# Performance work log

Measured on AMD Instinct MI355X. Metric: run time of the kernel, lower is better.

The kernel has to match this reference:

```python
import jax, jax.numpy as jnp
import numpy as np

# e2m1 FP4 lookup table (MXFP4)
FP4_VALUES = jnp.array([0.0, 0.5, 1.0, 1.5, 2.0, 3.0, 4.0, 6.0,
                        -0.0, -0.5, -1.0, -1.5, -2.0, -3.0, -4.0, -6.0], dtype=jnp.float32)
BLOCK = 32  # MXFP4/MXFP8 block size
SWIGLU_LIMIT = 7.0
SWIGLU_ALPHA = 1.702


def mxfp8_qdq(x):
    """Quantize-dequantize x to MXFP8: fp8_e4m3 mantissas with per-32-block E8M0 scales."""
    shp = x.shape
    nb = shp[-1] // BLOCK
    xb = x.reshape(*shp[:-1], nb, BLOCK)
    max_abs = jnp.max(jnp.abs(xb), axis=-1, keepdims=True)
    e = jnp.clip(jnp.ceil(jnp.log2(jnp.maximum(max_abs, 1e-12))), -127.0, 128.0)
    scale = jnp.exp2(e)
    xq = (xb / scale).astype(jnp.float8_e4m3fn).astype(x.dtype) * scale
    return xq.reshape(shp)


def dequant_mxfp4(blocks, scales):
    """blocks: [..., g, 16] int (packed nibbles), scales: [..., g] int (E8M0 biased 127).
    Returns [..., g*32] float32, low nibble first within each byte."""
    lo = FP4_VALUES[blocks & 15]
    hi = FP4_VALUES[blocks >> 4]
    vals = jnp.stack([lo, hi], axis=-1).reshape(*blocks.shape[:-1], BLOCK)  # interleave lo,hi
    e = (scales - 127).astype(jnp.float32)
    w = vals * jnp.exp2(e)[..., None]
    return w.reshape(*blocks.shape[:-2], blocks.shape[-2] * BLOCK)


def moe_forward(hidden_states, expert_indices, routing_weights,
                gate_up_blocks, gate_up_scales, gate_up_bias,
                down_blocks, down_scales, down_bias):
    w_gu = dequant_mxfp4(gate_up_blocks, gate_up_scales)  # [E, 2I, H]
    w_d = dequant_mxfp4(down_blocks, down_scales)          # [E, H, I]
    xq = mxfp8_qdq(hidden_states)                          # [T, H] mxfp8 qdq (row-blockwise)

    def one_expert(wgu, bgu, wd, bd):
        h = xq @ wgu.T + bgu                               # [T, 2I]
        gate = jnp.minimum(h[..., 0::2], SWIGLU_LIMIT)     # interleaved gate/up
        up = jnp.clip(h[..., 1::2], -SWIGLU_LIMIT, SWIGLU_LIMIT)
        glu = gate * jax.nn.sigmoid(SWIGLU_ALPHA * gate)
        act = (up + 1.0) * glu                             # [T, I]
        return mxfp8_qdq(act) @ wd.T + bd                  # [T, H]

    expert_outs = jax.vmap(one_expert)(w_gu, gate_up_bias, w_d, down_bias)  # [E, T, H]
    T = hidden_states.shape[0]
    sel = expert_outs[expert_indices, jnp.arange(T)[:, None]]  # [T, K, H]
    return jnp.sum(routing_weights[..., None] * sel, axis=1)   # [T, H]


def setup_inputs() -> dict:
    key = jax.random.key(0)
    ks = jax.random.split(key, 9)
    E, T, K, H, I = 8, 1024, 2, 2880, 2880
    return {
        'hidden_states': jax.random.normal(ks[0], (T, H), dtype=jnp.float32),
        'expert_indices': jax.random.randint(ks[1], (T, K), 0, E, dtype=jnp.int32),
        'routing_weights': jax.random.uniform(ks[2], (T, K), dtype=jnp.float32),
        'gate_up_blocks': jax.random.randint(ks[3], (E, 2 * I, H // 32, 16), 0, 256, dtype=jnp.int32),
        'gate_up_scales': jax.random.randint(ks[4], (E, 2 * I, H // 32), 0, 132, dtype=jnp.int32),
        'gate_up_bias': jax.random.normal(ks[5], (E, 2 * I), dtype=jnp.float32),
        'down_blocks': jax.random.randint(ks[6], (E, H, I // 32, 16), 0, 256, dtype=jnp.int32),
        'down_scales': jax.random.randint(ks[7], (E, H, I // 32), 0, 132, dtype=jnp.int32),
        'down_bias': jax.random.normal(ks[8], (E, H), dtype=jnp.float32),
    }


def reference(hidden_states, expert_indices, routing_weights,
              gate_up_blocks, gate_up_scales, gate_up_bias,
              down_blocks, down_scales, down_bias):
    return moe_forward(hidden_states, expert_indices, routing_weights,
                       gate_up_blocks, gate_up_scales, gate_up_bias,
                       down_blocks, down_scales, down_bias)
```

## Files before the change

kernel.cpp:

```cpp
#include <hip/hip_runtime.h>
#include <math.h>

#define T_TOK 1024
#define E_EXP 8
#define H_DIM 2880
#define I_DIM 2880
#define NGU   5760
#define KB    90
#define TM 128
#define TN 128
#define MAXROWS 3072

typedef __attribute__((ext_vector_type(8))) short short8;
typedef __attribute__((ext_vector_type(4))) float f32x4;

#define XQ_OFF   0ull
#define ACT_OFF  5898240ull
#define RTOK_OFF 23592960ull
#define RW_OFF   23605248ull
#define EB_OFF   23617536ull
#define EPC_OFF  23617600ull

__device__ inline ushort f2bf(float f) {
  unsigned u = __float_as_uint(f);
  unsigned r = u + 0x7FFFu + ((u >> 16) & 1u);
  return (ushort)(r >> 16);
}

__device__ inline int blk_exp(float amax) {
  amax = fmaxf(amax, 1e-12f);
  unsigned b = __float_as_uint(amax);
  int e = (int)(b >> 23) - 127;
  if (b & 0x7FFFFFu) e += 1;
  return min(max(e, -127), 128);
}

__device__ inline float qdq_val(float v, int eblk) {
  float av = fabsf(v);
  if (av == 0.f) return 0.f;
  int fl = (int)(__float_as_uint(av) >> 23) - 127 - eblk;
  int p = max(fl, -6) - 3;
  float step = ldexpf(1.f, p + eblk);
  return rintf(v / step) * step;
}

__device__ inline float fp4v(int n) {
  int mag = n & 7;
  float v;
  if (mag == 0) v = 0.f;
  else if (mag == 1) v = 0.5f;
  else v = ldexpf(1.0f + 0.5f * (float)(mag & 1), (mag >> 1) - 1);
  return (n & 8) ? -v : v;
}

__global__ void quant_x_kernel(const float* __restrict__ x, ushort* __restrict__ xq) {
  int g = blockIdx.x * 256 + threadIdx.x;
  float4 v4 = ((const float4*)x)[g];
  float am = fmaxf(fmaxf(fabsf(v4.x), fabsf(v4.y)), fmaxf(fabsf(v4.z), fabsf(v4.w)));
  am = fmaxf(am, __shfl_xor(am, 1));
  am = fmaxf(am, __shfl_xor(am, 2));
  am = fmaxf(am, __shfl_xor(am, 4));
  int eb = blk_exp(am);
  ushort4 o;
  o.x = f2bf(qdq_val(v4.x, eb));
  o.y = f2bf(qdq_val(v4.y, eb));
  o.z = f2bf(qdq_val(v4.z, eb));
  o.w = f2bf(qdq_val(v4.w, eb));
  ((ushort4*)xq)[g] = o;
}

__global__ void routing_kernel(const int* __restrict__ eidx, const float* __restrict__ rwt,
                               int* __restrict__ rtok, float* __restrict__ rw,
                               int* __restrict__ ebase, int* __restrict__ epc) {
  __shared__ int cnt[E_EXP];
  __shared__ int base_s[E_EXP];
  __shared__ int pos[E_EXP];
  int t = threadIdx.x;
  if (t < E_EXP) cnt[t] = 0;
  __syncthreads();
  for (int p = t; p < T_TOK * 2; p += 256) atomicAdd(&cnt[eidx[p]], 1);
  __syncthreads();
  if (t == 0) {
    int b = 0;
    for (int e = 0; e < E_EXP; e++) {
      base_s[e] = b;
      b += ((cnt[e] + TM - 1) / TM) * TM;
    }
  }
  __syncthreads();
  if (t < E_EXP) {
    pos[t] = 0;
    ebase[t] = base_s[t];
    epc[t] = ((cnt[t] + TM - 1) / TM) * TM;
  }
  __syncthreads();
  for (int p = t; p < T_TOK * 2; p += 256) {
    int e = eidx[p];
    int o = atomicAdd(&pos[e], 1);
    rtok[base_s[e] + o] = p >> 1;
    rw[base_s[e] + o] = rwt[p];
  }
  __syncthreads();
  for (int e = 0; e < E_EXP; e++) {
    int c = cnt[e], pc = ((c + TM - 1) / TM) * TM;
    for (int i = c + t; i < pc; i += 256) {
      rtok[base_s[e] + i] = 0;
      rw[base_s[e] + i] = 0.f;
    }
  }
}

__global__ __launch_bounds__(256, 2)
void gemm1_kernel(const ushort* __restrict__ xq,
                  const int* __restrict__ gub, const int* __restrict__ gus,
                  const float* __restrict__ gubias,
                  const int* __restrict__ rtok, const int* __restrict__ ebase,
                  const int* __restrict__ epc,
                  ushort* __restrict__ act) {
  const int ntile = blockIdx.x;
  const int e = blockIdx.y >> 4;
  const int mtile = blockIdx.y & 15;
  if (mtile * TM >= epc[e]) return;
  const int rowbase = ebase[e] + mtile * TM;

  __shared__ __align__(16) ushort lA[TM][40];
  __shared__ __align__(16) ushort lB[TN][40];
  __shared__ float2 lut[256];

  const int tid = threadIdx.x;
  lut[tid] = make_float2(fp4v(tid & 15), fp4v((tid >> 4) & 15));
  __syncthreads();

  const int wave = tid >> 6, lane = tid & 63;
  const int half = tid & 1, srow = tid >> 1;
  const int wm = (wave & 1) * 64, wn = (wave >> 1) * 64;
  const int lrow = lane & 15, q = lane >> 4;

  const int tokA = rtok[rowbase + srow];
  const ushort* aSrc = xq + tokA * H_DIM + half * 16;
  const int nrow = ntile * TN + srow;
  const int* bSrc = gub + ((e * NGU + nrow) * KB) * 16 + half * 8;
  const int* sSrc = gus + (e * NGU + nrow) * KB;

  f32x4 acc[4][4];
#pragma unroll
  for (int i = 0; i < 4; i++)
#pragma unroll
    for (int j = 0; j < 4; j++) acc[i][j] = (f32x4){0.f, 0.f, 0.f, 0.f};

  for (int kb = 0; kb < KB; kb++) {
    uint4 a0 = ((const uint4*)(aSrc + kb * 32))[0];
    uint4 a1 = ((const uint4*)(aSrc + kb * 32))[1];
    int4 b0 = ((const int4*)(bSrc + kb * 16))[0];
    int4 b1 = ((const int4*)(bSrc + kb * 16))[1];
    float sc = ldexpf(1.f, sSrc[kb] - 127);

    int bv[8] = {b0.x, b0.y, b0.z, b0.w, b1.x, b1.y, b1.z, b1.w};
    uint us[8];
#pragma unroll
    for (int j = 0; j < 8; j++) {
      float2 l = lut[bv[j] & 255];
      us[j] = (uint)f2bf(l.x * sc) | ((uint)f2bf(l.y * sc) << 16);
    }
    __syncthreads();
    *(uint4*)&lA[srow][half * 16] = a0;
    *(uint4*)&lA[srow][half * 16 + 8] = a1;
    uint4 w0; w0.x = us[0]; w0.y = us[1]; w0.z = us[2]; w0.w = us[3];
    uint4 w1; w1.x = us[4]; w1.y = us[5]; w1.z = us[6]; w1.w = us[7];
    *(uint4*)&lB[srow][half * 16] = w0;
    *(uint4*)&lB[srow][half * 16 + 8] = w1;
    __syncthreads();

    short8 af[4], bfr[4];
#pragma unroll
    for (int mi = 0; mi < 4; mi++) af[mi] = *(const short8*)&lA[wm + mi * 16 + lrow][q * 8];
#pragma unroll
    for (int ni = 0; ni < 4; ni++) bfr[ni] = *(const short8*)&lB[wn + ni * 16 + lrow][q * 8];
#pragma unroll
    for (int mi = 0; mi < 4; mi++)
#pragma unroll
      for (int ni = 0; ni < 4; ni++)
        acc[mi][ni] = __builtin_amdgcn_mfma_f32_16x16x32_bf16(af[mi], bfr[ni], acc[mi][ni], 0, 0, 0);
  }

  const int nbase = ntile * TN + wn;
  float bias_v[4];
#pragma unroll
  for (int ni = 0; ni < 4; ni++) bias_v[ni] = gubias[e * NGU + nbase + ni * 16 + lrow];
  const bool evenl = (lane & 1) == 0;
#pragma unroll
  for (int mi = 0; mi < 4; mi++) {
    float av[4][4];
#pragma unroll
    for (int ni = 0; ni < 4; ni++)
#pragma unroll
      for (int r = 0; r < 4; r++) {
        float h = acc[mi][ni][r] + bias_v[ni];
        float pp = __shfl_xor(h, 1);
        float gate = evenl ? h : pp;
        float up = evenl ? pp : h;
        gate = fminf(gate, 7.f);
        up = fminf(fmaxf(up, -7.f), 7.f);
        float glu = gate / (1.f + expf(-1.702f * gate));
        av[ni][r] = (up + 1.f) * glu;
      }
#pragma unroll
    for (int r = 0; r < 4; r++) {
      float am = 0.f;
#pragma unroll
      for (int ni = 0; ni < 4; ni++) am = fmaxf(am, fabsf(av[ni][r]));
      am = fmaxf(am, __shfl_xor(am, 2));
      am = fmaxf(am, __shfl_xor(am, 4));
      am = fmaxf(am, __shfl_xor(am, 8));
      int eb = blk_exp(am);
      if (evenl) {
        int row = rowbase + wm + mi * 16 + q * 4 + r;
        int cb = (nbase >> 1) + (lrow >> 1);
#pragma unroll
        for (int ni = 0; ni < 4; ni++)
          act[row * I_DIM + cb + ni * 8] = f2bf(qdq_val(av[ni][r], eb));
      }
    }
  }
}

__global__ __launch_bounds__(256, 2)
void gemm2_kernel(const ushort* __restrict__ act,
                  const int* __restrict__ db, const int* __restrict__ dsc,
                  const float* __restrict__ dbias,
                  const int* __restrict__ rtok, const float* __restrict__ rw,
                  const int* __restrict__ ebase, const int* __restrict__ epc,
                  float* __restrict__ out) {
  const int ntile = blockIdx.x;
  const int e = blockIdx.y >> 4;
  const int mtile = blockIdx.y & 15;
  if (mtile * TM >= epc[e]) return;
  const int rowbase = ebase[e] + mtile * TM;

  __shared__ __align__(16) ushort lA[TM][40];
  __shared__ __align__(16) ushort lB[TN][40];
  __shared__ float2 lut[256];

  const int tid = threadIdx.x;
  lut[tid] = make_float2(fp4v(tid & 15), fp4v((tid >> 4) & 15));
  __syncthreads();

  const int wave = tid >> 6, lane = tid & 63;
  const int half = tid & 1, srow = tid >> 1;
  const int wm = (wave & 1) * 64, wn = (wave >> 1) * 64;
  const int lrow = lane & 15, q = lane >> 4;

  const ushort* aSrc = act + (rowbase + srow) * I_DIM + half * 16;
  int nrow = ntile * TN + srow;
  if (nrow >= H_DIM) nrow = H_DIM - 1;
  const int* bSrc = db + ((e * H_DIM + nrow) * KB) * 16 + half * 8;
  const int* sSrc = dsc + (e * H_DIM + nrow) * KB;

  f32x4 acc[4][4];
#pragma unroll
  for (int i = 0; i < 4; i++)
#pragma unroll
    for (int j = 0; j < 4; j++) acc[i][j] = (f32x4){0.f, 0.f, 0.f, 0.f};

  for (int kb = 0; kb < KB; kb++) {
    uint4 a0 = ((const uint4*)(aSrc + kb * 32))[0];
    uint4 a1 = ((const uint4*)(aSrc + kb * 32))[1];
    int4 b0 = ((const int4*)(bSrc + kb * 16))[0];
    int4 b1 = ((const int4*)(bSrc + kb * 16))[1];
    float sc = ldexpf(1.f, sSrc[kb] - 127);

    int bv[8] = {b0.x, b0.y, b0.z, b0.w, b1.x, b1.y, b1.z, b1.w};
    uint us[8];
#pragma unroll
    for (int j = 0; j < 8; j++) {
      float2 l = lut[bv[j] & 255];
      us[j] = (uint)f2bf(l.x * sc) | ((uint)f2bf(l.y * sc) << 16);
    }
    __syncthreads();
    *(uint4*)&lA[srow][half * 16] = a0;
    *(uint4*)&lA[srow][half * 16 + 8] = a1;
    uint4 w0; w0.x = us[0]; w0.y = us[1]; w0.z = us[2]; w0.w = us[3];
    uint4 w1; w1.x = us[4]; w1.y = us[5]; w1.z = us[6]; w1.w = us[7];
    *(uint4*)&lB[srow][half * 16] = w0;
    *(uint4*)&lB[srow][half * 16 + 8] = w1;
    __syncthreads();

    short8 af[4], bfr[4];
#pragma unroll
    for (int mi = 0; mi < 4; mi++) af[mi] = *(const short8*)&lA[wm + mi * 16 + lrow][q * 8];
#pragma unroll
    for (int ni = 0; ni < 4; ni++) bfr[ni] = *(const short8*)&lB[wn + ni * 16 + lrow][q * 8];
#pragma unroll
    for (int mi = 0; mi < 4; mi++)
#pragma unroll
      for (int ni = 0; ni < 4; ni++)
        acc[mi][ni] = __builtin_amdgcn_mfma_f32_16x16x32_bf16(af[mi], bfr[ni], acc[mi][ni], 0, 0, 0);
  }

  const int nbase = ntile * TN + wn;
  float bias_v[4];
#pragma unroll
  for (int ni = 0; ni < 4; ni++) {
    int n = nbase + ni * 16 + lrow;
    bias_v[ni] = (n < H_DIM) ? dbias[e * H_DIM + n] : 0.f;
  }
#pragma unroll
  for (int mi = 0; mi < 4; mi++)
#pragma unroll
    for (int r = 0; r < 4; r++) {
      int orow = rowbase + wm + mi * 16 + q * 4 + r;
      int tok = rtok[orow];
      float w = rw[orow];
      if (w != 0.f) {
#pragma unroll
        for (int ni = 0; ni < 4; ni++) {
          int n = nbase + ni * 16 + lrow;
          if (n < H_DIM) atomicAdd(&out[tok * H_DIM + n], w * (acc[mi][ni][r] + bias_v[ni]));
        }
      }
    }
}

extern "C" void kernel_launch(void* const* d_in, const int* in_sizes, int n_in,
                              void* d_out, int out_size, void* d_ws, size_t ws_size,
                              hipStream_t stream) {
  const float* hs = (const float*)d_in[0];
  const int* eidx = (const int*)d_in[1];
  const float* rwt = (const float*)d_in[2];
  const int* gub = (const int*)d_in[3];
  const int* gus = (const int*)d_in[4];
  const float* gubias = (const float*)d_in[5];
  const int* db = (const int*)d_in[6];
  const int* dsc = (const int*)d_in[7];
  const float* dbias = (const float*)d_in[8];
  float* out = (float*)d_out;
  char* ws = (char*)d_ws;

  ushort* xq = (ushort*)(ws + XQ_OFF);
  ushort* act = (ushort*)(ws + ACT_OFF);
  int* rtok = (int*)(ws + RTOK_OFF);
  float* rw = (float*)(ws + RW_OFF);
  int* ebase = (int*)(ws + EB_OFF);
  int* epc = (int*)(ws + EPC_OFF);

  hipMemsetAsync(d_out, 0, (size_t)out_size * sizeof(float), stream);
  quant_x_kernel<<<2880, 256, 0, stream>>>(hs, xq);
  routing_kernel<<<1, 256, 0, stream>>>(eidx, rwt, rtok, rw, ebase, epc);
  gemm1_kernel<<<dim3(45, 128), 256, 0, stream>>>(xq, gub, gus, gubias, rtok, ebase, epc, act);
  gemm2_kernel<<<dim3(23, 128), 256, 0, stream>>>(act, db, dsc, dbias, rtok, rw, ebase, epc, out);
}
```

Before: 922.4 us.

## Prefetch next K-block into registers, simplify FP4 decode, split-K gemm2

Both GEMM kernels now load the next K-block's activations, packed weights and scale into registers while the current block is decoded and multiplied, to hide global load latency. FP4 decode packs bf16 halves with a byte permute instead of the f2bf conversion; this is exact because FP4 values times power-of-two scales fit in bf16. gemm2 is split along K into two halves via a third grid dimension, with bias added only by the first half, to raise parallelism for the small down-projection grid. The split doubles atomic adds to the output and register pressure rises from the prefetch buffers.

Result: faster. 810.4 us (-12.1%).

```diff
diff --git a/kernel.cpp b/kernel.cpp
--- a/kernel.cpp
+++ b/kernel.cpp
@@ -51,6 +51,13 @@
   else if (mag == 1) v = 0.5f;
   else v = ldexpf(1.0f + 0.5f * (float)(mag & 1), (mag >> 1) - 1);
   return (n & 8) ? -v : v;
+}
+
+__device__ inline uint dec_byte(const float2* lut, int b, float sc) {
+  float2 l = lut[b & 255];
+  uint lo = __float_as_uint(l.x * sc);
+  uint hi = __float_as_uint(l.y * sc);
+  return __builtin_amdgcn_perm(hi, lo, 0x07060302u);
 }
 
 __global__ void quant_x_kernel(const float* __restrict__ x, ushort* __restrict__ xq) {
@@ -148,20 +155,31 @@
 #pragma unroll
     for (int j = 0; j < 4; j++) acc[i][j] = (f32x4){0.f, 0.f, 0.f, 0.f};
 
+  uint4 a0 = ((const uint4*)(aSrc))[0];
+  uint4 a1 = ((const uint4*)(aSrc))[1];
+  int4 b0 = ((const int4*)(bSrc))[0];
+  int4 b1 = ((const int4*)(bSrc))[1];
+  int sraw = sSrc[0];
+
   for (int kb = 0; kb < KB; kb++) {
-    uint4 a0 = ((const uint4*)(aSrc + kb * 32))[0];
-    uint4 a1 = ((const uint4*)(aSrc + kb * 32))[1];
-    int4 b0 = ((const int4*)(bSrc + kb * 16))[0];
-    int4 b1 = ((const int4*)(bSrc + kb * 16))[1];
-    float sc = ldexpf(1.f, sSrc[kb] - 127);
-
-    int bv[8] = {b0.x, b0.y, b0.z, b0.w, b1.x, b1.y, b1.z, b1.w};
+    const int nk = (kb + 1 < KB) ? kb + 1 : kb;
+    uint4 na0 = ((const uint4*)(aSrc + nk * 32))[0];
+    uint4 na1 = ((const uint4*)(aSrc + nk * 32))[1];
+    int4 nb0 = ((const int4*)(bSrc + nk * 16))[0];
+    int4 nb1 = ((const int4*)(bSrc + nk * 16))[1];
+    int nsraw = sSrc[nk];
+
+    float sc = ldexpf(1.f, sraw - 127);
     uint us[8];
-#pragma unroll
-    for (int j = 0; j < 8; j++) {
-      float2 l = lut[bv[j] & 255];
-      us[j] = (uint)f2bf(l.x * sc) | ((uint)f2bf(l.y * sc) << 16);
-    }
+    us[0] = dec_byte(lut, b0.x, sc);
+    us[1] = dec_byte(lut, b0.y, sc);
+    us[2] = dec_byte(lut, b0.z, sc);
+    us[3] = dec_byte(lut, b0.w, sc);
+    us[4] = dec_byte(lut, b1.x, sc);
+    us[5] = dec_byte(lut, b1.y, sc);
+    us[6] = dec_byte(lut, b1.z, sc);
+    us[7] = dec_byte(lut, b1.w, sc);
+
     __syncthreads();
     *(uint4*)&lA[srow][half * 16] = a0;
     *(uint4*)&lA[srow][half * 16 + 8] = a1;
@@ -181,6 +199,8 @@
 #pragma unroll
       for (int ni = 0; ni < 4; ni++)
         acc[mi][ni] = __builtin_amdgcn_mfma_f32_16x16x32_bf16(af[mi], bfr[ni], acc[mi][ni], 0, 0, 0);
+
+    a0 = na0; a1 = na1; b0 = nb0; b1 = nb1; sraw = nsraw;
   }
 
   const int nbase = ntile * TN + wn;
@@ -236,6 +256,8 @@
   const int mtile = blockIdx.y & 15;
   if (mtile * TM >= epc[e]) return;
   const int rowbase = ebase[e] + mtile * TM;
+  const int kz = blockIdx.z;
+  const int kb0 = kz * (KB / 2), kb1 = kb0 + (KB / 2);
 
   __shared__ __align__(16) ushort lA[TM][40];
   __shared__ __align__(16) ushort lB[TN][40];
@@ -262,20 +284,31 @@
 #pragma unroll
     for (int j = 0; j < 4; j++) acc[i][j] = (f32x4){0.f, 0.f, 0.f, 0.f};
 
-  for (int kb = 0; kb < KB; kb++) {
-    uint4 a0 = ((const uint4*)(aSrc + kb * 32))[0];
-    uint4 a1 = ((const uint4*)(aSrc + kb * 32))[1];
-    int4 b0 = ((const int4*)(bSrc + kb * 16))[0];
-    int4 b1 = ((const int4*)(bSrc + kb * 16))[1];
-    float sc = ldexpf(1.f, sSrc[kb] - 127);
-
-    int bv[8] = {b0.x, b0.y, b0.z, b0.w, b1.x, b1.y, b1.z, b1.w};
+  uint4 a0 = ((const uint4*)(aSrc + kb0 * 32))[0];
+  uint4 a1 = ((const uint4*)(aSrc + kb0 * 32))[1];
+  int4 b0 = ((const int4*)(bSrc + kb0 * 16))[0];
+  int4 b1 = ((const int4*)(bSrc + kb0 * 16))[1];
+  int sraw = sSrc[kb0];
+
+  for (int kb = kb0; kb < kb1; kb++) {
+    const int nk = (kb + 1 < kb1) ? kb + 1 : kb;
+    uint4 na0 = ((const uint4*)(aSrc + nk * 32))[0];
+    uint4 na1 = ((const uint4*)(aSrc + nk * 32))[1];
+    int4 nb0 = ((const int4*)(bSrc + nk * 16))[0];
+    int4 nb1 = ((const int4*)(bSrc + nk * 16))[1];
+    int nsraw = sSrc[nk];
+
+    float sc = ldexpf(1.f, sraw - 127);
     uint us[8];
-#pragma unroll
-    for (int j = 0; j < 8; j++) {
-      float2 l = lut[bv[j] & 255];
-      us[j] = (uint)f2bf(l.x * sc) | ((uint)f2bf(l.y * sc) << 16);
-    }
+    us[0] = dec_byte(lut, b0.x, sc);
+    us[1] = dec_byte(lut, b0.y, sc);
+    us[2] = dec_byte(lut, b0.z, sc);
+    us[3] = dec_byte(lut, b0.w, sc);
+    us[4] = dec_byte(lut, b1.x, sc);
+    us[5] = dec_byte(lut, b1.y, sc);
+    us[6] = dec_byte(lut, b1.z, sc);
+    us[7] = dec_byte(lut, b1.w, sc);
+
     __syncthreads();
     *(uint4*)&lA[srow][half * 16] = a0;
     *(uint4*)&lA[srow][half * 16 + 8] = a1;
@@ -295,6 +328,8 @@
 #pragma unroll
       for (int ni = 0; ni < 4; ni++)
         acc[mi][ni] = __builtin_amdgcn_mfma_f32_16x16x32_bf16(af[mi], bfr[ni], acc[mi][ni], 0, 0, 0);
+
+    a0 = na0; a1 = na1; b0 = nb0; b1 = nb1; sraw = nsraw;
   }
 
   const int nbase = ntile * TN + wn;
@@ -302,7 +337,7 @@
 #pragma unroll
   for (int ni = 0; ni < 4; ni++) {
     int n = nbase + ni * 16 + lrow;
-    bias_v[ni] = (n < H_DIM) ? dbias[e * H_DIM + n] : 0.f;
+    bias_v[ni] = (kz == 0 && n < H_DIM) ? dbias[e * H_DIM + n] : 0.f;
   }
 #pragma unroll
   for (int mi = 0; mi < 4; mi++)
@@ -347,5 +382,5 @@
   quant_x_kernel<<<2880, 256, 0, stream>>>(hs, xq);
   routing_kernel<<<1, 256, 0, stream>>>(eidx, rwt, rtok, rw, ebase, epc);
   gemm1_kernel<<<dim3(45, 128), 256, 0, stream>>>(xq, gub, gus, gubias, rtok, ebase, epc, act);
-  gemm2_kernel<<<dim3(23, 128), 256, 0, stream>>>(act, db, dsc, dbias, rtok, rw, ebase, epc, out);
-}
+  gemm2_kernel<<<dim3(23, 128, 2), 256, 0, stream>>>(act, db, dsc, dbias, rtok, rw, ebase, epc, out);
+}
```

## Repack int32 MXFP4 weights to bytes, decode via byte-permute tables, split-K gemm2

Applied to the files above, without the earlier changes.

Adds a repack pass that compresses the int32-per-byte weight and scale arrays into packed bytes, so the GEMM kernels read a quarter of the weight traffic. New gemm kernels decode FP4 nibbles to bf16 by truncation with v_perm table lookups instead of an LDS LUT plus rounding, and register-prefetch the next K step. gemm2 is split along K in two halves combined through the existing atomics. The repack runs on every call, and bf16 truncation is exact only because the scaled FP4 values fit in bf16.

Result: faster. 816.6 us (-11.5%).

```diff
diff --git a/kernel.cpp b/kernel.cpp
--- a/kernel.cpp
+++ b/kernel.cpp
@@ -14,12 +14,19 @@
 typedef __attribute__((ext_vector_type(8))) short short8;
 typedef __attribute__((ext_vector_type(4))) float f32x4;
 
+#define PERM(a, b, s) __builtin_amdgcn_perm((uint)(a), (uint)(b), (uint)(s))
+
 #define XQ_OFF   0ull
 #define ACT_OFF  5898240ull
 #define RTOK_OFF 23592960ull
 #define RW_OFF   23605248ull
 #define EB_OFF   23617536ull
-#define EPC_OFF  23617600ull
+#define EPC_OFF  23617568ull
+#define CGU_OFF  23617664ull
+#define CGS_OFF  89972864ull
+#define CDB_OFF  94120064ull
+#define CDS_OFF  127297664ull
+#define WS_NEED  129371264ull
 
 __device__ inline ushort f2bf(float f) {
   unsigned u = __float_as_uint(f);
@@ -51,6 +58,75 @@
   else if (mag == 1) v = 0.5f;
   else v = ldexpf(1.0f + 0.5f * (float)(mag & 1), (mag >> 1) - 1);
   return (n & 8) ? -v : v;
+}
+
+__device__ inline uint dec_byte(const float2* lut, int b, float sc) {
+  float2 l = lut[b & 255];
+  uint lo = __float_as_uint(l.x * sc);
+  uint hi = __float_as_uint(l.y * sc);
+  return PERM(hi, lo, 0x07060302u);
+}
+
+struct BTbl { uint tlo_l, tlo_h, thi_l, thi_h; };
+
+__device__ inline BTbl build_tbl(float sc) {
+  uint g0 = 0u;
+  uint g1 = __float_as_uint(0.5f * sc);
+  uint g2 = __float_as_uint(sc);
+  uint g3 = __float_as_uint(1.5f * sc);
+  uint g4 = __float_as_uint(2.0f * sc);
+  uint g5 = __float_as_uint(3.0f * sc);
+  uint g6 = __float_as_uint(4.0f * sc);
+  uint g7 = __float_as_uint(6.0f * sc);
+  uint p01 = PERM(g1, g0, 0x07030602u);
+  uint p23 = PERM(g3, g2, 0x07030602u);
+  uint p45 = PERM(g5, g4, 0x07030602u);
+  uint p67 = PERM(g7, g6, 0x07030602u);
+  BTbl t;
+  t.tlo_l = PERM(p23, p01, 0x05040100u);
+  t.thi_l = PERM(p23, p01, 0x07060302u);
+  t.tlo_h = PERM(p67, p45, 0x05040100u);
+  t.thi_h = PERM(p67, p45, 0x07060302u);
+  return t;
+}
+
+__device__ inline uint4 dec_w(uint w, const BTbl& t) {
+  uint ml = w & 0x07070707u;
+  uint mh = (w >> 4) & 0x07070707u;
+  uint sl = (w << 4) & 0x80808080u;
+  uint sh = w & 0x80808080u;
+  uint hl = PERM(t.thi_h, t.thi_l, ml) | sl;
+  uint hh = PERM(t.thi_h, t.thi_l, mh) | sh;
+  uint ll = PERM(t.tlo_h, t.tlo_l, ml);
+  uint lh = PERM(t.tlo_h, t.tlo_l, mh);
+  uint4 o;
+  o.x = PERM(hl, ll, 0x05010400u);
+  o.y = PERM(hl, ll, 0x07030602u);
+  o.z = PERM(hh, lh, 0x05010400u);
+  o.w = PERM(hh, lh, 0x07030602u);
+  return o;
+}
+
+__device__ inline uint4 aperm(uint4 u) {
+  uint4 v;
+  v.x = PERM(u.y, u.x, 0x05040100u);
+  v.y = PERM(u.w, u.z, 0x05040100u);
+  v.z = PERM(u.y, u.x, 0x07060302u);
+  v.w = PERM(u.w, u.z, 0x07060302u);
+  return v;
+}
+
+__global__ void repack_kernel(const int* __restrict__ src, uint4* __restrict__ dst, int n16) {
+  int g = blockIdx.x * 256 + threadIdx.x;
+  if (g >= n16) return;
+  const int4* s = (const int4*)(src) + g * 4;
+  int4 w0 = s[0], w1 = s[1], w2 = s[2], w3 = s[3];
+  uint4 o;
+  o.x = (uint)(w0.x & 255) | ((uint)(w0.y & 255) << 8) | ((uint)(w0.z & 255) << 16) | ((uint)(w0.w) << 24);
+  o.y = (uint)(w1.x & 255) | ((uint)(w1.y & 255) << 8) | ((uint)(w1.z & 255) << 16) | ((uint)(w1.w) << 24);
+  o.z = (uint)(w2.x & 255) | ((uint)(w2.y & 255) << 8) | ((uint)(w2.z & 255) << 16) | ((uint)(w2.w) << 24);
+  o.w = (uint)(w3.x & 255) | ((uint)(w3.y & 255) << 8) | ((uint)(w3.z & 255) << 16) | ((uint)(w3.w) << 24);
+  dst[g] = o;
 }
 
 __global__ void quant_x_kernel(const float* __restrict__ x, ushort* __restrict__ xq) {
@@ -111,6 +187,221 @@
 }
 
 __global__ __launch_bounds__(256, 2)
+void gemm1c_kernel(const ushort* __restrict__ xq,
+                   const uchar* __restrict__ cgu, const uchar* __restrict__ cgs,
+                   const float* __restrict__ gubias,
+                   const int* __restrict__ rtok, const int* __restrict__ ebase,
+                   const int* __restrict__ epc,
+                   ushort* __restrict__ act) {
+  const int ntile = blockIdx.x;
+  const int e = blockIdx.y >> 4;
+  const int mtile = blockIdx.y & 15;
+  if (mtile * TM >= epc[e]) return;
+  const int rowbase = ebase[e] + mtile * TM;
+
+  __shared__ __align__(16) ushort lA[TM][40];
+  __shared__ __align__(16) ushort lB[TN][40];
+
+  const int tid = threadIdx.x;
+  const int wave = tid >> 6, lane = tid & 63;
+  const int half = tid & 1, srow = tid >> 1;
+  const int wm = (wave & 1) * 64, wn = (wave >> 1) * 64;
+  const int lrow = lane & 15, q = lane >> 4;
+
+  const int tokA = rtok[rowbase + srow];
+  const ushort* aSrc = xq + tokA * H_DIM + half * 16;
+  const int nrow = ntile * TN + srow;
+  const uchar* bSrc = cgu + (size_t)(e * NGU + nrow) * 1440 + half * 8;
+  const uchar* sSrc = cgs + (size_t)(e * NGU + nrow) * KB;
+
+  f32x4 acc[4][4];
+#pragma unroll
+  for (int i = 0; i < 4; i++)
+#pragma unroll
+    for (int j = 0; j < 4; j++) acc[i][j] = (f32x4){0.f, 0.f, 0.f, 0.f};
+
+  uint4 a0 = ((const uint4*)(aSrc))[0];
+  uint4 a1 = ((const uint4*)(aSrc))[1];
+  uint2 bw = *(const uint2*)(bSrc);
+  uchar sb = sSrc[0];
+
+  for (int kb = 0; kb < KB; kb++) {
+    const int nk = (kb + 1 < KB) ? kb + 1 : kb;
+    uint4 na0 = ((const uint4*)(aSrc + nk * 32))[0];
+    uint4 na1 = ((const uint4*)(aSrc + nk * 32))[1];
+    uint2 nbw = *(const uint2*)(bSrc + nk * 16);
+    uchar nsb = sSrc[nk];
+
+    float sc = ldexpf(1.f, (int)sb - 127);
+    BTbl t = build_tbl(sc);
+    uint4 d0 = dec_w(bw.x, t);
+    uint4 d1 = dec_w(bw.y, t);
+    uint4 pa0 = aperm(a0);
+    uint4 pa1 = aperm(a1);
+
+    __syncthreads();
+    *(uint4*)&lA[srow][half * 16] = pa0;
+    *(uint4*)&lA[srow][half * 16 + 8] = pa1;
+    *(uint4*)&lB[srow][half * 16] = d0;
+    *(uint4*)&lB[srow][half * 16 + 8] = d1;
+    __syncthreads();
+
+    short8 af[4], bfr[4];
+#pragma unroll
+    for (int mi = 0; mi < 4; mi++) af[mi] = *(const short8*)&lA[wm + mi * 16 + lrow][q * 8];
+#pragma unroll
+    for (int ni = 0; ni < 4; ni++) bfr[ni] = *(const short8*)&lB[wn + ni * 16 + lrow][q * 8];
+#pragma unroll
+    for (int mi = 0; mi < 4; mi++)
+#pragma unroll
+      for (int ni = 0; ni < 4; ni++)
+        acc[mi][ni] = __builtin_amdgcn_mfma_f32_16x16x32_bf16(af[mi], bfr[ni], acc[mi][ni], 0, 0, 0);
+
+    a0 = na0; a1 = na1; bw = nbw; sb = nsb;
+  }
+
+  const int nbase = ntile * TN + wn;
+  float bias_v[4];
+#pragma unroll
+  for (int ni = 0; ni < 4; ni++) bias_v[ni] = gubias[e * NGU + nbase + ni * 16 + lrow];
+  const bool evenl = (lane & 1) == 0;
+#pragma unroll
+  for (int mi = 0; mi < 4; mi++) {
+    float av[4][4];
+#pragma unroll
+    for (int ni = 0; ni < 4; ni++)
+#pragma unroll
+      for (int r = 0; r < 4; r++) {
+        float h = acc[mi][ni][r] + bias_v[ni];
+        float pp = __shfl_xor(h, 1);
+        float gate = evenl ? h : pp;
+        float up = evenl ? pp : h;
+        gate = fminf(gate, 7.f);
+        up = fminf(fmaxf(up, -7.f), 7.f);
+        float glu = gate / (1.f + expf(-1.702f * gate));
+        av[ni][r] = (up + 1.f) * glu;
+      }
+#pragma unroll
+    for (int r = 0; r < 4; r++) {
+      float am = 0.f;
+#pragma unroll
+      for (int ni = 0; ni < 4; ni++) am = fmaxf(am, fabsf(av[ni][r]));
+      am = fmaxf(am, __shfl_xor(am, 2));
+      am = fmaxf(am, __shfl_xor(am, 4));
+      am = fmaxf(am, __shfl_xor(am, 8));
+      int eb = blk_exp(am);
+      if (evenl) {
+        int row = rowbase + wm + mi * 16 + q * 4 + r;
+        int cb = (nbase >> 1) + (lrow >> 1);
+#pragma unroll
+        for (int ni = 0; ni < 4; ni++)
+          act[row * I_DIM + cb + ni * 8] = f2bf(qdq_val(av[ni][r], eb));
+      }
+    }
+  }
+}
+
+__global__ __launch_bounds__(256, 2)
+void gemm2c_kernel(const ushort* __restrict__ act,
+                   const uchar* __restrict__ cdb, const uchar* __restrict__ cds,
+                   const float* __restrict__ dbias,
+                   const int* __restrict__ rtok, const float* __restrict__ rw,
+                   const int* __restrict__ ebase, const int* __restrict__ epc,
+                   float* __restrict__ out) {
+  const int ntile = blockIdx.x;
+  const int e = blockIdx.y >> 4;
+  const int mtile = blockIdx.y & 15;
+  if (mtile * TM >= epc[e]) return;
+  const int rowbase = ebase[e] + mtile * TM;
+  const int kz = blockIdx.z;
+  const int kb0 = kz * (KB / 2), kb1 = kb0 + (KB / 2);
+
+  __shared__ __align__(16) ushort lA[TM][40];
+  __shared__ __align__(16) ushort lB[TN][40];
+
+  const int tid = threadIdx.x;
+  const int wave = tid >> 6, lane = tid & 63;
+  const int half = tid & 1, srow = tid >> 1;
+  const int wm = (wave & 1) * 64, wn = (wave >> 1) * 64;
+  const int lrow = lane & 15, q = lane >> 4;
+
+  const ushort* aSrc = act + (size_t)(rowbase + srow) * I_DIM + half * 16;
+  int nrow = ntile * TN + srow;
+  if (nrow >= H_DIM) nrow = H_DIM - 1;
+  const uchar* bSrc = cdb + (size_t)(e * H_DIM + nrow) * 1440 + half * 8;
+  const uchar* sSrc = cds + (size_t)(e * H_DIM + nrow) * KB;
+
+  f32x4 acc[4][4];
+#pragma unroll
+  for (int i = 0; i < 4; i++)
+#pragma unroll
+    for (int j = 0; j < 4; j++) acc[i][j] = (f32x4){0.f, 0.f, 0.f, 0.f};
+
+  uint4 a0 = ((const uint4*)(aSrc + kb0 * 32))[0];
+  uint4 a1 = ((const uint4*)(aSrc + kb0 * 32))[1];
+  uint2 bw = *(const uint2*)(bSrc + kb0 * 16);
+  uchar sb = sSrc[kb0];
+
+  for (int kb = kb0; kb < kb1; kb++) {
+    const int nk = (kb + 1 < kb1) ? kb + 1 : kb;
+    uint4 na0 = ((const uint4*)(aSrc + nk * 32))[0];
+    uint4 na1 = ((const uint4*)(aSrc + nk * 32))[1];
+    uint2 nbw = *(const uint2*)(bSrc + nk * 16);
+    uchar nsb = sSrc[nk];
+
+    float sc = ldexpf(1.f, (int)sb - 127);
+    BTbl t = build_tbl(sc);
+    uint4 d0 = dec_w(bw.x, t);
+    uint4 d1 = dec_w(bw.y, t);
+    uint4 pa0 = aperm(a0);
+    uint4 pa1 = aperm(a1);
+
+    __syncthreads();
+    *(uint4*)&lA[srow][half * 16] = pa0;
+    *(uint4*)&lA[srow][half * 16 + 8] = pa1;
+    *(uint4*)&lB[srow][half * 16] = d0;
+    *(uint4*)&lB[srow][half * 16 + 8] = d1;
+    __syncthreads();
+
+    short8 af[4], bfr[4];
+#pragma unroll
+    for (int mi = 0; mi < 4; mi++) af[mi] = *(const short8*)&lA[wm + mi * 16 + lrow][q * 8];
+#pragma unroll
+    for (int ni = 0; ni < 4; ni++) bfr[ni] = *(const short8*)&lB[wn + ni * 16 + lrow][q * 8];
+#pragma unroll
+    for (int mi = 0; mi < 4; mi++)
+#pragma unroll
+      for (int ni = 0; ni < 4; ni++)
+        acc[mi][ni] = __builtin_amdgcn_mfma_f32_16x16x32_bf16(af[mi], bfr[ni], acc[mi][ni], 0, 0, 0);
+
+    a0 = na0; a1 = na1; bw = nbw; sb = nsb;
+  }
+
+  const int nbase = ntile * TN + wn;
+  float bias_v[4];
+#pragma unroll
+  for (int ni = 0; ni < 4; ni++) {
+    int n = nbase + ni * 16 + lrow;
+    bias_v[ni] = (kz == 0 && n < H_DIM) ? dbias[e * H_DIM + n] : 0.f;
+  }
+#pragma unroll
+  for (int mi = 0; mi < 4; mi++)
+#pragma unroll
+    for (int r = 0; r < 4; r++) {
+      int orow = rowbase + wm + mi * 16 + q * 4 + r;
+      int tok = rtok[orow];
+      float w = rw[orow];
+      if (w != 0.f) {
+#pragma unroll
+        for (int ni = 0; ni < 4; ni++) {
+          int n = nbase + ni * 16 + lrow;
+          if (n < H_DIM) atomicAdd(&out[tok * H_DIM + n], w * (acc[mi][ni][r] + bias_v[ni]));
+        }
+      }
+    }
+}
+
+__global__ __launch_bounds__(256, 2)
 void gemm1_kernel(const ushort* __restrict__ xq,
                   const int* __restrict__ gub, const int* __restrict__ gus,
                   const float* __restrict__ gubias,
@@ -154,14 +445,10 @@
     int4 b0 = ((const int4*)(bSrc + kb * 16))[0];
     int4 b1 = ((const int4*)(bSrc + kb * 16))[1];
     float sc = ldexpf(1.f, sSrc[kb] - 127);
-
     int bv[8] = {b0.x, b0.y, b0.z, b0.w, b1.x, b1.y, b1.z, b1.w};
     uint us[8];
 #pragma unroll
-    for (int j = 0; j < 8; j++) {
-      float2 l = lut[bv[j] & 255];
-      us[j] = (uint)f2bf(l.x * sc) | ((uint)f2bf(l.y * sc) << 16);
-    }
+    for (int j = 0; j < 8; j++) us[j] = dec_byte(lut, bv[j], sc);
     __syncthreads();
     *(uint4*)&lA[srow][half * 16] = a0;
     *(uint4*)&lA[srow][half * 16 + 8] = a1;
@@ -170,7 +457,6 @@
     *(uint4*)&lB[srow][half * 16] = w0;
     *(uint4*)&lB[srow][half * 16 + 8] = w1;
     __syncthreads();
-
     short8 af[4], bfr[4];
 #pragma unroll
     for (int mi = 0; mi < 4; mi++) af[mi] = *(const short8*)&lA[wm + mi * 16 + lrow][q * 8];
@@ -236,6 +522,8 @@
   const int mtile = blockIdx.y & 15;
   if (mtile * TM >= epc[e]) return;
   const int rowbase = ebase[e] + mtile * TM;
+  const int kz = blockIdx.z;
+  const int kb0 = kz * (KB / 2), kb1 = kb0 + (KB / 2);
 
   __shared__ __align__(16) ushort lA[TM][40];
   __shared__ __align__(16) ushort lB[TN][40];
@@ -262,20 +550,16 @@
 #pragma unroll
     for (int j = 0; j < 4; j++) acc[i][j] = (f32x4){0.f, 0.f, 0.f, 0.f};
 
-  for (int kb = 0; kb < KB; kb++) {
+  for (int kb = kb0; kb < kb1; kb++) {
     uint4 a0 = ((const uint4*)(aSrc + kb * 32))[0];
     uint4 a1 = ((const uint4*)(aSrc + kb * 32))[1];
     int4 b0 = ((const int4*)(bSrc + kb * 16))[0];
     int4 b1 = ((const int4*)(bSrc + kb * 16))[1];
     float sc = ldexpf(1.f, sSrc[kb] - 127);
-
     int bv[8] = {b0.x, b0.y, b0.z, b0.w, b1.x, b1.y, b1.z, b1.w};
     uint us[8];
 #pragma unroll
-    for (int j = 0; j < 8; j++) {
-      float2 l = lut[bv[j] & 255];
-      us[j] = (uint)f2bf(l.x * sc) | ((uint)f2bf(l.y * sc) << 16);
-    }
+    for (int j = 0; j < 8; j++) us[j] = dec_byte(lut, bv[j], sc);
     __syncthreads();
     *(uint4*)&lA[srow][half * 16] = a0;
     *(uint4*)&lA[srow][half * 16 + 8] = a1;
@@ -284,7 +568,6 @@
     *(uint4*)&lB[srow][half * 16] = w0;
     *(uint4*)&lB[srow][half * 16 + 8] = w1;
     __syncthreads();
-
     short8 af[4], bfr[4];
 #pragma unroll
     for (int mi = 0; mi < 4; mi++) af[mi] = *(const short8*)&lA[wm + mi * 16 + lrow][q * 8];
@@ -302,7 +585,7 @@
 #pragma unroll
   for (int ni = 0; ni < 4; ni++) {
     int n = nbase + ni * 16 + lrow;
-    bias_v[ni] = (n < H_DIM) ? dbias[e * H_DIM + n] : 0.f;
+    bias_v[ni] = (kz == 0 && n < H_DIM) ? dbias[e * H_DIM + n] : 0.f;
   }
 #pragma unroll
   for (int mi = 0; mi < 4; mi++)
@@ -346,6 +629,20 @@
   hipMemsetAsync(d_out, 0, (size_t)out_size * sizeof(float), stream);
   quant_x_kernel<<<2880, 256, 0, stream>>>(hs, xq);
   routing_kernel<<<1, 256, 0, stream>>>(eidx, rwt, rtok, rw, ebase, epc);
-  gemm1_kernel<<<dim3(45, 128), 256, 0, stream>>>(xq, gub, gus, gubias, rtok, ebase, epc, act);
-  gemm2_kernel<<<dim3(23, 128), 256, 0, stream>>>(act, db, dsc, dbias, rtok, rw, ebase, epc, out);
-}
+
+  if (ws_size >= WS_NEED) {
+    uchar* cgu = (uchar*)(ws + CGU_OFF);
+    uchar* cgs = (uchar*)(ws + CGS_OFF);
+    uchar* cdb = (uchar*)(ws + CDB_OFF);
+    uchar* cds = (uchar*)(ws + CDS_OFF);
+    repack_kernel<<<16200, 256, 0, stream>>>(gub, (uint4*)cgu, 4147200);
+    repack_kernel<<<8100, 256, 0, stream>>>(db, (uint4*)cdb, 2073600);
+    repack_kernel<<<1013, 256, 0, stream>>>(gus, (uint4*)cgs, 259200);
+    repack_kernel<<<507, 256, 0, stream>>>(dsc, (uint4*)cds, 129600);
+    gemm1c_kernel<<<dim3(45, 128), 256, 0, stream>>>(xq, cgu, cgs, gubias, rtok, ebase, epc, act);
+    gemm2c_kernel<<<dim3(23, 128, 2), 256, 0, stream>>>(act, cdb, cds, dbias, rtok, rw, ebase, epc, out);
+  } else {
+    gemm1_kernel<<<dim3(45, 128), 256, 0, stream>>>(xq, gub, gus, gubias, rtok, ebase, epc, act);
+    gemm2_kernel<<<dim3(23, 128, 2), 256, 0, stream>>>(act, db, dsc, dbias, rtok, rw, ebase, epc, out);
+  }
+}
```
